# Optimization experiments

Hardware: AMD Instinct MI355X
Metric: run time of the kernel (lower is better)

The kernel has to match this reference:

```python
import jax, jax.numpy as jnp
import numpy as np

# Material constants (from init_kwargs: E=1e4, nu=0.3)
E_MOD = 1.0e4
NU = 0.3
MU = E_MOD / (2.0 * (1.0 + NU))                      # shear modulus
LMBDA = E_MOD * NU / ((1.0 + NU) * (1.0 - 2.0 * NU))  # first Lame parameter
EPS = 1e-10

B, N_NODES, N_ELEM, N_QUAD, NPE = 4, 100000, 500000, 4, 4  # tet4 mesh


def setup_inputs() -> dict:
    key = jax.random.key(0)
    k1, k2, k3, k4 = jax.random.split(key, 4)
    # small displacements so J = det(I + grad_u) stays positive
    u = jax.random.normal(k1, (B, N_NODES, 3), dtype=jnp.float32) * 0.01
    elements = jax.random.randint(k2, (N_ELEM, NPE), 0, N_NODES)
    # precomputed shape-function derivatives dN/dx per element/quad point
    dN_dx = jax.random.normal(k3, (N_ELEM, N_QUAD, NPE, 3), dtype=jnp.float32) * 0.1
    # positive Jacobian determinants of the reference->physical map
    detJ = jax.random.uniform(k4, (N_ELEM, N_QUAD), dtype=jnp.float32, minval=0.5, maxval=1.5) * 1e-3
    # tet4 4-point quadrature weights: 0.25 / 6
    quad_weights = jnp.full((N_QUAD,), 0.25 / 6.0, dtype=jnp.float32)
    return {"u": u, "elements": elements, "dN_dx": dN_dx, "detJ": detJ,
            "quad_weights": quad_weights}


def reference(u, elements, dN_dx, detJ, quad_weights):
    # gather nodal displacements per element: [B, E, n, 3]
    elem_u = u[:, elements]
    # grad_u[b,e,q,i,j] = sum_n elem_u[b,e,n,i] * dN_dx[e,q,n,j]  -> [B,E,Q,3,3]
    grad_u = jnp.einsum('beni,eqnj->beqij', elem_u, dN_dx)
    F = grad_u + jnp.eye(3, dtype=u.dtype)
    J = jnp.linalg.det(F)                      # [B,E,Q]
    I_C = jnp.sum(F * F, axis=(-2, -1))        # tr(F^T F)
    logJ = jnp.log(jnp.maximum(J, EPS))
    W = 0.5 * MU * (I_C - 3.0 - 2.0 * logJ) + 0.25 * LMBDA * (J * J - 1.0 - 2.0 * logJ)
    # quadrature-weighted assembly over elements and quad points -> [B]
    return jnp.einsum('beq,eq,q->b', W, detJ, quad_weights)
```

## Files before the change

### kernel.cpp

```cpp
#include <hip/hip_runtime.h>

#define MU_C   3846.1538461538462f
#define LM_C   5769.2307692307695f
#define EPS_C  1e-10f


__global__ __launch_bounds__(256) void nh_transpose_u(
    const float* __restrict__ u, float* __restrict__ ut, int n_nodes)
{
    const int i = blockIdx.x * 256 + threadIdx.x;
    if (i >= n_nodes) return;
    float v[4][3];
    #pragma unroll
    for (int b = 0; b < 4; ++b) {
        const float* p = u + ((size_t)b * n_nodes + i) * 3;
        v[b][0] = p[0]; v[b][1] = p[1]; v[b][2] = p[2];
    }
    float4* q4 = reinterpret_cast<float4*>(ut + (size_t)i * 12);
    q4[0] = make_float4(v[0][0], v[0][1], v[0][2], v[1][0]);
    q4[1] = make_float4(v[1][1], v[1][2], v[2][0], v[2][1]);
    q4[2] = make_float4(v[2][2], v[3][0], v[3][1], v[3][2]);
}

__global__ __launch_bounds__(256) void nh_partial_eb(
    const float* __restrict__ u,
    const float* __restrict__ ut,
    const int*   __restrict__ elements,
    const float* __restrict__ dN_dx,
    const float* __restrict__ detJ,
    const float* __restrict__ qw,
    float* __restrict__ partial,
    int n_elem, int n_nodes, int use_ut)
{
    const int t = blockIdx.x * 256 + threadIdx.x;
    const int e = t >> 2;
    const int b = t & 3;

    float a = 0.f;

    if (e < n_elem) {
        const int4 nd = *reinterpret_cast<const int4*>(elements + (size_t)e * 4);
        const int nodes[4] = {nd.x, nd.y, nd.z, nd.w};

        float4 dv[12];
        const float4* dp = reinterpret_cast<const float4*>(dN_dx) + (size_t)e * 12;
        #pragma unroll
        for (int k = 0; k < 12; ++k) dv[k] = dp[k];
        const float* d = reinterpret_cast<const float*>(dv);

        const float4 dj = reinterpret_cast<const float4*>(detJ)[e];
        const float4 w4 = *reinterpret_cast<const float4*>(qw);
        const float wq[4] = {dj.x * w4.x, dj.y * w4.y, dj.z * w4.z, dj.w * w4.w};

        float eu[4][3];
        if (use_ut) {
            const float* ub = ut + b * 3;
            #pragma unroll
            for (int n = 0; n < 4; ++n) {
                const float* p = ub + nodes[n] * 12;
                eu[n][0] = p[0]; eu[n][1] = p[1]; eu[n][2] = p[2];
            }
        } else {
            const float* ub = u + (size_t)b * n_nodes * 3;
            #pragma unroll
            for (int n = 0; n < 4; ++n) {
                const float* p = ub + nodes[n] * 3;
                eu[n][0] = p[0]; eu[n][1] = p[1]; eu[n][2] = p[2];
            }
        }

        #pragma unroll
        for (int q = 0; q < 4; ++q) {
            float F[3][3];
            #pragma unroll
            for (int i = 0; i < 3; ++i) {
                #pragma unroll
                for (int j = 0; j < 3; ++j) {
                    float g = 0.f;
                    #pragma unroll
                    for (int n = 0; n < 4; ++n)
                        g = fmaf(eu[n][i], d[(q*4 + n)*3 + j], g);
                    F[i][j] = g + ((i == j) ? 1.f : 0.f);
                }
            }
            const float J =
                  F[0][0] * (F[1][1]*F[2][2] - F[1][2]*F[2][1])
                - F[0][1] * (F[1][0]*F[2][2] - F[1][2]*F[2][0])
                + F[0][2] * (F[1][0]*F[2][1] - F[1][1]*F[2][0]);

            float IC = 0.f;
            #pragma unroll
            for (int i = 0; i < 3; ++i)
                #pragma unroll
                for (int j = 0; j < 3; ++j)
                    IC = fmaf(F[i][j], F[i][j], IC);

            const float lj = __logf(fmaxf(J, EPS_C));
            const float W = 0.5f * MU_C * (IC - 3.f - 2.f * lj)
                          + 0.25f * LM_C * (fmaf(J, J, -1.f) - 2.f * lj);
            a = fmaf(W, wq[q], a);
        }
    }

    #pragma unroll
    for (int off = 32; off >= 4; off >>= 1)
        a += __shfl_down(a, off);

    __shared__ float lds[4][4];
    const int lane = threadIdx.x & 63;
    const int wid  = threadIdx.x >> 6;
    if (lane < 4) lds[wid][lane] = a;
    __syncthreads();
    if (threadIdx.x < 4)
        partial[(size_t)blockIdx.x * 4 + threadIdx.x] =
            (lds[0][threadIdx.x] + lds[1][threadIdx.x]) +
            (lds[2][threadIdx.x] + lds[3][threadIdx.x]);
}

__global__ __launch_bounds__(256) void nh_final(
    const float* __restrict__ partial,
    float* __restrict__ out,
    int nparts)
{
    float accb[4] = {0.f, 0.f, 0.f, 0.f};
    for (int i = threadIdx.x; i < nparts; i += 256) {
        const float4 p = reinterpret_cast<const float4*>(partial)[i];
        accb[0] += p.x; accb[1] += p.y; accb[2] += p.z; accb[3] += p.w;
    }

    #pragma unroll
    for (int b = 0; b < 4; ++b) {
        float v = accb[b];
        #pragma unroll
        for (int off = 32; off > 0; off >>= 1)
            v += __shfl_down(v, off);
        accb[b] = v;
    }

    __shared__ float lds[4][4];
    const int lane = threadIdx.x & 63;
    const int wid  = threadIdx.x >> 6;
    if (lane == 0) {
        #pragma unroll
        for (int b = 0; b < 4; ++b) lds[wid][b] = accb[b];
    }
    __syncthreads();
    if (threadIdx.x == 0) {
        #pragma unroll
        for (int b = 0; b < 4; ++b)
            out[b] = (lds[0][b] + lds[1][b]) + (lds[2][b] + lds[3][b]);
    }
}

extern "C" void kernel_launch(void* const* d_in, const int* in_sizes, int n_in,
                              void* d_out, int out_size, void* d_ws, size_t ws_size,
                              hipStream_t stream) {
    const float* u        = (const float*)d_in[0];
    const int*   elements = (const int*)d_in[1];
    const float* dN_dx    = (const float*)d_in[2];
    const float* detJ     = (const float*)d_in[3];
    const float* qw       = (const float*)d_in[4];
    float* out = (float*)d_out;

    const int B       = out_size;
    const int n_nodes = in_sizes[0] / (3 * B);
    const int n_elem  = in_sizes[1] / 4;

    const int threads = 256;
    const int n_thr   = n_elem * 4;
    const int nblocks = (n_thr + threads - 1) / threads;

    const size_t ut_bytes      = (size_t)n_nodes * 48;
    const size_t partial_bytes = (size_t)nblocks * 4 * sizeof(float);
    const int use_ut = (ws_size >= ut_bytes + partial_bytes) ? 1 : 0;

    float* ut      = (float*)d_ws;
    float* partial = use_ut ? (float*)((char*)d_ws + ut_bytes) : (float*)d_ws;

    if (use_ut) {
        const int tb = (n_nodes + threads - 1) / threads;
        nh_transpose_u<<<tb, threads, 0, stream>>>(u, ut, n_nodes);
    }

    nh_partial_eb<<<nblocks, threads, 0, stream>>>(u, ut, elements, dN_dx, detJ, qw,
                                                   partial, n_elem, n_nodes, use_ut);
    nh_final<<<1, threads, 0, stream>>>(partial, out, nblocks);
}
```

Before: 58.92 us.

## Stage per-element dN_dx in LDS with coalesced loads, pad node layout to float4

The element kernel now loads each 64-element block's dN_dx, connectivity and detJ into shared memory with coalesced float4 loads. Before, each of the 4 batch threads for an element read the same 192 bytes of dN_dx on its own with strided accesses. The transposed displacement buffer is padded to one float4 per node per batch, so each gather is a single aligned 16-byte load. This costs more shared memory per block, an extra barrier, and a larger workspace (64 vs 48 bytes per node), which also raises the size needed before the transposed path is used.

```diff
diff --git a/kernel.cpp b/kernel.cpp
--- a/kernel.cpp
+++ b/kernel.cpp
@@ -4,27 +4,25 @@
 #define LM_C   5769.2307692307695f
 #define EPS_C  1e-10f
 
-
-__global__ __launch_bounds__(256) void nh_transpose_u(
-    const float* __restrict__ u, float* __restrict__ ut, int n_nodes)
+#define ELB 64
+#define SLAB 52
+
+__global__ __launch_bounds__(256) void nh_transpose_u_pad(
+    const float* __restrict__ u, float4* __restrict__ ut, int n_nodes)
 {
     const int i = blockIdx.x * 256 + threadIdx.x;
     if (i >= n_nodes) return;
-    float v[4][3];
+    float4* q = ut + (size_t)i * 4;
     #pragma unroll
     for (int b = 0; b < 4; ++b) {
         const float* p = u + ((size_t)b * n_nodes + i) * 3;
-        v[b][0] = p[0]; v[b][1] = p[1]; v[b][2] = p[2];
-    }
-    float4* q4 = reinterpret_cast<float4*>(ut + (size_t)i * 12);
-    q4[0] = make_float4(v[0][0], v[0][1], v[0][2], v[1][0]);
-    q4[1] = make_float4(v[1][1], v[1][2], v[2][0], v[2][1]);
-    q4[2] = make_float4(v[2][2], v[3][0], v[3][1], v[3][2]);
-}
-
-__global__ __launch_bounds__(256) void nh_partial_eb(
+        q[b] = make_float4(p[0], p[1], p[2], 0.f);
+    }
+}
+
+__global__ __launch_bounds__(256) void nh_partial_v3(
     const float* __restrict__ u,
-    const float* __restrict__ ut,
+    const float4* __restrict__ ut,
     const int*   __restrict__ elements,
     const float* __restrict__ dN_dx,
     const float* __restrict__ detJ,
@@ -32,45 +30,77 @@
     float* __restrict__ partial,
     int n_elem, int n_nodes, int use_ut)
 {
-    const int t = blockIdx.x * 256 + threadIdx.x;
-    const int e = t >> 2;
-    const int b = t & 3;
-
+    __shared__ float s_dn[ELB * SLAB];
+    __shared__ int   s_el[ELB * 4];
+    __shared__ float s_dj[ELB * 4];
+    __shared__ float s_red[4][4];
+
+    const int t  = threadIdx.x;
+    const int e0 = blockIdx.x * ELB;
+    const int rem = min(ELB, n_elem - e0);
+
+    {
+        const float4* src = reinterpret_cast<const float4*>(dN_dx) + (size_t)e0 * 12;
+        const int nf4 = rem * 12;
+        #pragma unroll
+        for (int j = 0; j < 3; ++j) {
+            const int m = t + 256 * j;
+            if (m < nf4) {
+                const float4 v = src[m];
+                const int el = m / 12, ch = m % 12;
+                *reinterpret_cast<float4*>(&s_dn[el * SLAB + ch * 4]) = v;
+            }
+        }
+    }
+    if (t < 64) {
+        if (t < rem)
+            reinterpret_cast<int4*>(s_el)[t] =
+                reinterpret_cast<const int4*>(elements)[e0 + t];
+    } else if (t < 128) {
+        const int i = t - 64;
+        if (i < rem)
+            reinterpret_cast<float4*>(s_dj)[i] =
+                reinterpret_cast<const float4*>(detJ)[e0 + i];
+    }
+    __syncthreads();
+
+    const int el = t >> 2;
+    const int b  = t & 3;
     float a = 0.f;
 
-    if (e < n_elem) {
-        const int4 nd = *reinterpret_cast<const int4*>(elements + (size_t)e * 4);
+    if (el < rem) {
+        const int4 nd = reinterpret_cast<const int4*>(s_el)[el];
         const int nodes[4] = {nd.x, nd.y, nd.z, nd.w};
-
-        float4 dv[12];
-        const float4* dp = reinterpret_cast<const float4*>(dN_dx) + (size_t)e * 12;
-        #pragma unroll
-        for (int k = 0; k < 12; ++k) dv[k] = dp[k];
-        const float* d = reinterpret_cast<const float*>(dv);
-
-        const float4 dj = reinterpret_cast<const float4*>(detJ)[e];
-        const float4 w4 = *reinterpret_cast<const float4*>(qw);
-        const float wq[4] = {dj.x * w4.x, dj.y * w4.y, dj.z * w4.z, dj.w * w4.w};
 
         float eu[4][3];
         if (use_ut) {
-            const float* ub = ut + b * 3;
             #pragma unroll
             for (int n = 0; n < 4; ++n) {
-                const float* p = ub + nodes[n] * 12;
-                eu[n][0] = p[0]; eu[n][1] = p[1]; eu[n][2] = p[2];
+                const float4 v = ut[(size_t)nodes[n] * 4 + b];
+                eu[n][0] = v.x; eu[n][1] = v.y; eu[n][2] = v.z;
             }
         } else {
             const float* ub = u + (size_t)b * n_nodes * 3;
             #pragma unroll
             for (int n = 0; n < 4; ++n) {
-                const float* p = ub + nodes[n] * 3;
+                const float* p = ub + (size_t)nodes[n] * 3;
                 eu[n][0] = p[0]; eu[n][1] = p[1]; eu[n][2] = p[2];
             }
         }
 
+        const float4 w4 = *reinterpret_cast<const float4*>(qw);
+        const float* dj = &s_dj[el * 4];
+        const float wq[4] = {dj[0] * w4.x, dj[1] * w4.y, dj[2] * w4.z, dj[3] * w4.w};
+
+        const float* slab = &s_dn[el * SLAB];
         #pragma unroll
         for (int q = 0; q < 4; ++q) {
+            float4 f0 = *reinterpret_cast<const float4*>(slab + q * 12 + 0);
+            float4 f1 = *reinterpret_cast<const float4*>(slab + q * 12 + 4);
+            float4 f2 = *reinterpret_cast<const float4*>(slab + q * 12 + 8);
+            float d[12] = {f0.x, f0.y, f0.z, f0.w, f1.x, f1.y, f1.z, f1.w,
+                           f2.x, f2.y, f2.z, f2.w};
+
             float F[3][3];
             #pragma unroll
             for (int i = 0; i < 3; ++i) {
@@ -79,7 +109,7 @@
                     float g = 0.f;
                     #pragma unroll
                     for (int n = 0; n < 4; ++n)
-                        g = fmaf(eu[n][i], d[(q*4 + n)*3 + j], g);
+                        g = fmaf(eu[n][i], d[n * 3 + j], g);
                     F[i][j] = g + ((i == j) ? 1.f : 0.f);
                 }
             }
@@ -106,15 +136,13 @@
     for (int off = 32; off >= 4; off >>= 1)
         a += __shfl_down(a, off);
 
-    __shared__ float lds[4][4];
-    const int lane = threadIdx.x & 63;
-    const int wid  = threadIdx.x >> 6;
-    if (lane < 4) lds[wid][lane] = a;
+    const int lane = t & 63;
+    const int wid  = t >> 6;
+    if (lane < 4) s_red[wid][lane] = a;
     __syncthreads();
-    if (threadIdx.x < 4)
-        partial[(size_t)blockIdx.x * 4 + threadIdx.x] =
-            (lds[0][threadIdx.x] + lds[1][threadIdx.x]) +
-            (lds[2][threadIdx.x] + lds[3][threadIdx.x]);
+    if (t < 4)
+        partial[(size_t)blockIdx.x * 4 + t] =
+            (s_red[0][t] + s_red[1][t]) + (s_red[2][t] + s_red[3][t]);
 }
 
 __global__ __launch_bounds__(256) void nh_final(
@@ -167,22 +195,21 @@
     const int n_elem  = in_sizes[1] / 4;
 
     const int threads = 256;
-    const int n_thr   = n_elem * 4;
-    const int nblocks = (n_thr + threads - 1) / threads;
-
-    const size_t ut_bytes      = (size_t)n_nodes * 48;
+    const int nblocks = (n_elem + ELB - 1) / ELB;
+
+    const size_t ut_bytes      = (size_t)n_nodes * 4 * sizeof(float4);
     const size_t partial_bytes = (size_t)nblocks * 4 * sizeof(float);
     const int use_ut = (ws_size >= ut_bytes + partial_bytes) ? 1 : 0;
 
-    float* ut      = (float*)d_ws;
+    float4* ut     = (float4*)d_ws;
     float* partial = use_ut ? (float*)((char*)d_ws + ut_bytes) : (float*)d_ws;
 
     if (use_ut) {
         const int tb = (n_nodes + threads - 1) / threads;
-        nh_transpose_u<<<tb, threads, 0, stream>>>(u, ut, n_nodes);
-    }
-
-    nh_partial_eb<<<nblocks, threads, 0, stream>>>(u, ut, elements, dN_dx, detJ, qw,
+        nh_transpose_u_pad<<<tb, threads, 0, stream>>>(u, ut, n_nodes);
+    }
+
+    nh_partial_v3<<<nblocks, threads, 0, stream>>>(u, ut, elements, dN_dx, detJ, qw,
                                                    partial, n_elem, n_nodes, use_ut);
     nh_final<<<1, threads, 0, stream>>>(partial, out, nblocks);
 }
```

Result: no change. 59.97 us (+1.8%).
